# Kernel optimization log

Measured on AMD Instinct MI355X. Metric: run time of the kernel, lower is better.

Reference implementation:

```python
import jax, jax.numpy as jnp
import numpy as np

EPS = 0.5          # entropy_epsilon
TAU = 0.5          # tau = 1 * entropy_epsilon
MAXITER = 10

NABLA_W = np.array([[[[0., 0., 0.], [0., -1., 0.], [0., 1., 0.]]],
                    [[[0., 0., 0.], [0., -1., 1.], [0., 0., 0.]]]], dtype=np.float32)  # (2,1,3,3)
DIV_W = np.array([[[[0., -1., 0.], [0., 1., 0.], [0., 0., 0.]],
                   [[0., 0., 0.], [-1., 1., 0.], [0., 0., 0.]]]], dtype=np.float32)    # (1,2,3,3)


def _conv(x, w):
    # x: (B,C,H,W), w: (O,I,3,3), padding=1 -> SAME
    return jax.lax.conv_general_dilated(
        x, w, window_strides=(1, 1), padding='SAME',
        dimension_numbers=('NCHW', 'OIHW', 'NCHW'))


def setup_inputs() -> dict:
    key = jax.random.key(0)
    k1, k2 = jax.random.split(key)
    B, H, W = 8, 1024, 1024
    o = jax.random.normal(k1, (B, 1, H, W), dtype=jnp.float32)
    vector_field = jax.random.normal(k2, (H, W, 2), dtype=jnp.float32)
    nabla_w = jnp.asarray(NABLA_W)
    div_w = jnp.asarray(DIV_W)
    return {"o": o, "vector_field": vector_field, "nabla_w": nabla_w, "div_w": div_w}


def reference(o, vector_field, nabla_w, div_w):
    o = o[:, 0]                      # (B,H,W)
    vf1 = vector_field[:, :, 1]      # (H,W)
    vf0 = vector_field[:, :, 0]      # (H,W)
    u = jax.nn.sigmoid(o / EPS)
    q = jnp.zeros_like(o)
    Tq = jnp.zeros_like(o)
    for _ in range(MAXITER):
        u_nabla = _conv(u[:, None], nabla_w)          # (B,2,H,W)
        q = q - TAU * (u_nabla[:, 0] * vf1 + u_nabla[:, 1] * vf0)
        q = jnp.maximum(q, 0.0)
        Tq = _conv(jnp.stack([vf1 * q, vf0 * q], axis=1), div_w)[:, 0]  # (B,H,W)
        u = jax.nn.sigmoid((o - Tq) / EPS)
    u1 = (o - Tq) / EPS
    return u1
```

## Files before the change

kernel.cpp:

```cpp
#include <hip/hip_runtime.h>
#include <math.h>

#define IMG_H 1024
#define IMG_W 1024
#define IMG_B 8
#define TPB 1024
#define RPB 16
#define BANDS (IMG_H / RPB)
#define NBLK (IMG_B * BANDS)

__device__ __forceinline__ float sig2(float x) {
    return 1.0f / (1.0f + __expf(-2.0f * x));
}
__device__ __forceinline__ int imax(int a, int b) { return a > b ? a : b; }
__device__ __forceinline__ int imin(int a, int b) { return a < b ? a : b; }

template<int D, bool READQ, bool FINAL>
__global__ __launch_bounds__(TPB, 8) void k_pipe(const float* __restrict__ qin,
                                                 const float* __restrict__ vf,
                                                 const float* __restrict__ o,
                                                 float* __restrict__ out) {
    __shared__ float sp[2][TPB + 1];
    __shared__ float su[D][2][TPB + 1];

    const int img = blockIdx.x / BANDS;
    const int r0  = (blockIdx.x % BANDS) * RPB;
    const int tid = threadIdx.x;
    const size_t ibase = (size_t)img * IMG_H * IMG_W;

    if (tid == 0) {
        sp[0][0] = 0.0f; sp[1][0] = 0.0f;
#pragma unroll
        for (int l = 0; l < D; ++l) { su[l][0][TPB] = 0.0f; su[l][1][TPB] = 0.0f; }
    }

    constexpr int HALO = FINAL ? 1 : 0;
    constexpr int NOH  = FINAL ? D + 1 : D;

    const int u0lo = imax(r0 - (D - 1) - HALO, 0);
    const int ylo  = READQ ? imax(r0 - D - HALO, 0) : u0lo;
    const int yend = r0 + RPB - 1 + D;
    const int yhi  = imin(yend, IMG_H - 1);

    float qc = 0.0f, qz = 0.0f;
    float oh[NOH];
    float v0h[D + 1], v1h[D + 1];
    float uY[D], uZ[D];
    float p1prev[D + 1];
    float qsave[D];
    float qvPrev = 0.0f;

#pragma unroll
    for (int l = 0; l < NOH; ++l) oh[l] = 0.0f;
#pragma unroll
    for (int l = 0; l <= D; ++l) { v0h[l] = 0.0f; v1h[l] = 0.0f; p1prev[l] = 0.0f; }
#pragma unroll
    for (int l = 0; l < D; ++l) { uY[l] = 0.0f; uZ[l] = 0.0f; qsave[l] = 0.0f; }

    const float* pQ = qin + ibase + (size_t)ylo * IMG_W + tid;
    const float* pO = o   + ibase + (size_t)ylo * IMG_W + tid;
    const float* pV = vf  + ((size_t)ylo * IMG_W + tid) * 2;

    for (int y = ylo; y <= yend; ++y) {
#pragma unroll
        for (int k = NOH - 1; k >= 1; --k) oh[k] = oh[k - 1];
#pragma unroll
        for (int k = D; k >= 1; --k) { v0h[k] = v0h[k - 1]; v1h[k] = v1h[k - 1]; }
        if constexpr (READQ) qz = qc;

        if (y <= yhi) {
            if constexpr (READQ) { qc = *pQ; pQ += IMG_W; }
            oh[0] = *pO; pO += IMG_W;
            float2 v2 = *(const float2*)pV; pV += 2 * IMG_W;
            v0h[0] = v2.x; v1h[0] = v2.y;
        } else {
            qc = 0.0f; oh[0] = 0.0f; v0h[0] = 0.0f; v1h[0] = 0.0f;
        }

        if constexpr (READQ) {
            float p0c = v0h[0] * qc;
            float p1c = v1h[0] * qc;
            sp[0][tid + 1] = p0c;
            __syncthreads();
            if (y >= u0lo) {
                float pm1 = sp[0][tid];
                float nu = (y <= IMG_H - 1)
                    ? sig2(oh[0] - (p1c - p1prev[0] + p0c - pm1)) : 0.0f;
                uZ[0] = uY[0]; uY[0] = nu;
                su[0][y & 1][tid] = nu;
            }
            p1prev[0] = p1c;
        } else {
            float nu = (y <= IMG_H - 1) ? sig2(oh[0]) : 0.0f;
            uZ[0] = uY[0]; uY[0] = nu;
            su[0][y & 1][tid] = nu;
        }

#pragma unroll
        for (int l = 1; l <= D; ++l) {
            const int t = y - l;
            const int qlo = imax(r0 - (D - l) - HALO, 0);
            const bool qvalid = (t >= qlo) && (t <= IMG_H - 1);
            float qbase = (l == 1) ? (READQ ? qz : 0.0f) : qsave[l - 1];
            if (l >= 2) qsave[l - 1] = qvPrev;
            float qv;
            if (qvalid) {
                const float uR = su[l - 1][t & 1][tid + 1];
                float gy = uY[l - 1] - uZ[l - 1];
                float gx = uR - uZ[l - 1];
                qv = fmaxf(qbase - 0.5f * (gy * v1h[l] + gx * v0h[l]), 0.0f);
            } else {
                qv = 0.0f;
            }

            if (l < D) {
                float p0p = v0h[l] * qv;
                float p1p = v1h[l] * qv;
                sp[l & 1][tid + 1] = p0p;
                __syncthreads();
                const int ulo = imax(r0 - (D - 1 - l) - HALO, 0);
                if (t >= ulo) {
                    float pm1 = sp[l & 1][tid];
                    float nu = (t <= IMG_H - 1)
                        ? sig2(oh[l] - (p1p - p1prev[l] + p0p - pm1)) : 0.0f;
                    uZ[l] = uY[l]; uY[l] = nu;
                    su[l][t & 1][tid] = nu;
                }
                p1prev[l] = p1p;
            } else {
                if constexpr (FINAL) {
                    float p0p = v0h[D] * qv;
                    float p1p = v1h[D] * qv;
                    sp[D & 1][tid + 1] = p0p;
                    __syncthreads();
                    if (t >= r0 && t < r0 + RPB) {
                        float pm1 = sp[D & 1][tid];
                        float Tq = p1p - p1prev[D] + p0p - pm1;
                        out[ibase + (size_t)t * IMG_W + tid] = 2.0f * (oh[D] - Tq);
                    }
                    p1prev[D] = p1p;
                } else {
                    if (t >= r0 && t < r0 + RPB)
                        out[ibase + (size_t)t * IMG_W + tid] = qv;
                }
            }
            qvPrev = qv;
        }
    }
}

extern "C" void kernel_launch(void* const* d_in, const int* in_sizes, int n_in,
                              void* d_out, int out_size, void* d_ws, size_t ws_size,
                              hipStream_t stream) {
    const float* o  = (const float*)d_in[0];
    const float* vf = (const float*)d_in[1];
    float* qA = (float*)d_ws;

    k_pipe<5, false, false><<<NBLK, TPB, 0, stream>>>(o, vf, o, qA);
    k_pipe<5, true,  true ><<<NBLK, TPB, 0, stream>>>(qA, vf, o, (float*)d_out);
}
```

Baseline: 218.0 us.

## Replace block-wide shared-memory exchange with wavefront-local shuffles over overlapping column strips

Each block now holds two 64-lane wavefronts, and each wavefront covers an overlapping 128-column strip (stride 116, horizontal halo of 6). Neighbour values are exchanged with __shfl_up/__shfl_down instead of shared memory, and each lane handles two pixels with float2/float4 loads. This removes the many __syncthreads per row across a 1024-thread block. The cost is redundant halo computation, about 10% extra work per strip, and more registers per thread.

```diff
diff --git a/kernel.cpp b/kernel.cpp
--- a/kernel.cpp
+++ b/kernel.cpp
@@ -4,10 +4,14 @@
 #define IMG_H 1024
 #define IMG_W 1024
 #define IMG_B 8
-#define TPB 1024
+#define TPB 128
 #define RPB 16
 #define BANDS (IMG_H / RPB)
-#define NBLK (IMG_B * BANDS)
+#define NSTR 9
+#define STRIDE 116
+#define XHALO 6
+#define WPB (TPB / 64)
+#define NBLK (IMG_B * BANDS * NSTR / WPB)
 
 __device__ __forceinline__ float sig2(float x) {
     return 1.0f / (1.0f + __expf(-2.0f * x));
@@ -16,23 +20,22 @@
 __device__ __forceinline__ int imin(int a, int b) { return a < b ? a : b; }
 
 template<int D, bool READQ, bool FINAL>
-__global__ __launch_bounds__(TPB, 8) void k_pipe(const float* __restrict__ qin,
+__global__ __launch_bounds__(TPB, 4) void k_pipe(const float* __restrict__ qin,
                                                  const float* __restrict__ vf,
                                                  const float* __restrict__ o,
                                                  float* __restrict__ out) {
-    __shared__ float sp[2][TPB + 1];
-    __shared__ float su[D][2][TPB + 1];
-
-    const int img = blockIdx.x / BANDS;
-    const int r0  = (blockIdx.x % BANDS) * RPB;
-    const int tid = threadIdx.x;
+    const int gw    = blockIdx.x * WPB + (threadIdx.x >> 6);
+    const int strip = gw % NSTR;
+    const int bg    = gw / NSTR;
+    const int band  = bg % BANDS;
+    const int img   = bg / BANDS;
+    const int lane  = threadIdx.x & 63;
+    const int r0    = band * RPB;
+    const int x     = strip * STRIDE - XHALO + lane * 2;
+    const bool ok   = ((unsigned)x < (unsigned)IMG_W);
+    const int  xc   = imin(imax(x, 0), IMG_W - 2);
+    const bool inter = ok && (lane >= 3) && (lane <= 60);
     const size_t ibase = (size_t)img * IMG_H * IMG_W;
-
-    if (tid == 0) {
-        sp[0][0] = 0.0f; sp[1][0] = 0.0f;
-#pragma unroll
-        for (int l = 0; l < D; ++l) { su[l][0][TPB] = 0.0f; su[l][1][TPB] = 0.0f; }
-    }
 
     constexpr int HALO = FINAL ? 1 : 0;
     constexpr int NOH  = FINAL ? D + 1 : D;
@@ -42,58 +45,77 @@
     const int yend = r0 + RPB - 1 + D;
     const int yhi  = imin(yend, IMG_H - 1);
 
-    float qc = 0.0f, qz = 0.0f;
-    float oh[NOH];
-    float v0h[D + 1], v1h[D + 1];
-    float uY[D], uZ[D];
-    float p1prev[D + 1];
-    float qsave[D];
-    float qvPrev = 0.0f;
+    float qc[2], qz[2], qvPrev[2];
+    float oh[NOH][2];
+    float v0h[D + 1][2], v1h[D + 1][2];
+    float uY[D][2], uZ[D][2];
+    float p1prev[D + 1][2];
+    float qsave[D][2];
 
 #pragma unroll
-    for (int l = 0; l < NOH; ++l) oh[l] = 0.0f;
+    for (int j = 0; j < 2; ++j) {
+        qc[j] = qz[j] = qvPrev[j] = 0.0f;
 #pragma unroll
-    for (int l = 0; l <= D; ++l) { v0h[l] = 0.0f; v1h[l] = 0.0f; p1prev[l] = 0.0f; }
+        for (int l = 0; l < NOH; ++l) oh[l][j] = 0.0f;
 #pragma unroll
-    for (int l = 0; l < D; ++l) { uY[l] = 0.0f; uZ[l] = 0.0f; qsave[l] = 0.0f; }
+        for (int l = 0; l <= D; ++l) { v0h[l][j] = 0.0f; v1h[l][j] = 0.0f; p1prev[l][j] = 0.0f; }
+#pragma unroll
+        for (int l = 0; l < D; ++l) { uY[l][j] = 0.0f; uZ[l][j] = 0.0f; qsave[l][j] = 0.0f; }
+    }
 
-    const float* pQ = qin + ibase + (size_t)ylo * IMG_W + tid;
-    const float* pO = o   + ibase + (size_t)ylo * IMG_W + tid;
-    const float* pV = vf  + ((size_t)ylo * IMG_W + tid) * 2;
+    const float* pQ = qin + ibase + (size_t)ylo * IMG_W + xc;
+    const float* pO = o   + ibase + (size_t)ylo * IMG_W + xc;
+    const float* pV = vf  + ((size_t)ylo * IMG_W + xc) * 2;
 
     for (int y = ylo; y <= yend; ++y) {
 #pragma unroll
-        for (int k = NOH - 1; k >= 1; --k) oh[k] = oh[k - 1];
+        for (int k = NOH - 1; k >= 1; --k) { oh[k][0] = oh[k-1][0]; oh[k][1] = oh[k-1][1]; }
 #pragma unroll
-        for (int k = D; k >= 1; --k) { v0h[k] = v0h[k - 1]; v1h[k] = v1h[k - 1]; }
-        if constexpr (READQ) qz = qc;
+        for (int k = D; k >= 1; --k) {
+            v0h[k][0] = v0h[k-1][0]; v0h[k][1] = v0h[k-1][1];
+            v1h[k][0] = v1h[k-1][0]; v1h[k][1] = v1h[k-1][1];
+        }
+        if constexpr (READQ) { qz[0] = qc[0]; qz[1] = qc[1]; }
 
         if (y <= yhi) {
-            if constexpr (READQ) { qc = *pQ; pQ += IMG_W; }
-            oh[0] = *pO; pO += IMG_W;
-            float2 v2 = *(const float2*)pV; pV += 2 * IMG_W;
-            v0h[0] = v2.x; v1h[0] = v2.y;
+            if constexpr (READQ) {
+                float2 q2 = *(const float2*)pQ; pQ += IMG_W;
+                qc[0] = q2.x; qc[1] = q2.y;
+            }
+            float2 o2 = *(const float2*)pO; pO += IMG_W;
+            oh[0][0] = ok ? o2.x : -1e30f;
+            oh[0][1] = ok ? o2.y : -1e30f;
+            float4 v4 = *(const float4*)pV; pV += 2 * IMG_W;
+            v0h[0][0] = ok ? v4.x : 0.0f;  v1h[0][0] = ok ? v4.y : 0.0f;
+            v0h[0][1] = ok ? v4.z : 0.0f;  v1h[0][1] = ok ? v4.w : 0.0f;
         } else {
-            qc = 0.0f; oh[0] = 0.0f; v0h[0] = 0.0f; v1h[0] = 0.0f;
+            qc[0] = qc[1] = 0.0f;
+            oh[0][0] = oh[0][1] = 0.0f;
+            v0h[0][0] = v0h[0][1] = 0.0f;
+            v1h[0][0] = v1h[0][1] = 0.0f;
         }
 
         if constexpr (READQ) {
-            float p0c = v0h[0] * qc;
-            float p1c = v1h[0] * qc;
-            sp[0][tid + 1] = p0c;
-            __syncthreads();
+            float p0c[2], p1c[2];
+            p0c[0] = v0h[0][0] * qc[0];  p0c[1] = v0h[0][1] * qc[1];
+            p1c[0] = v1h[0][0] * qc[0];  p1c[1] = v1h[0][1] * qc[1];
+            const float pm1 = __shfl_up(p0c[1], 1);
             if (y >= u0lo) {
-                float pm1 = sp[0][tid];
-                float nu = (y <= IMG_H - 1)
-                    ? sig2(oh[0] - (p1c - p1prev[0] + p0c - pm1)) : 0.0f;
-                uZ[0] = uY[0]; uY[0] = nu;
-                su[0][y & 1][tid] = nu;
+#pragma unroll
+                for (int j = 0; j < 2; ++j) {
+                    float pl = (j == 0) ? pm1 : p0c[0];
+                    float arg = oh[0][j] - (p1c[j] - p1prev[0][j] + p0c[j] - pl);
+                    float nu = (y <= IMG_H - 1) ? sig2(arg) : 0.0f;
+                    uZ[0][j] = uY[0][j]; uY[0][j] = nu;
+                }
             }
-            p1prev[0] = p1c;
+            p1prev[0][0] = p1c[0]; p1prev[0][1] = p1c[1];
         } else {
-            float nu = (y <= IMG_H - 1) ? sig2(oh[0]) : 0.0f;
-            uZ[0] = uY[0]; uY[0] = nu;
-            su[0][y & 1][tid] = nu;
+#pragma unroll
+            for (int j = 0; j < 2; ++j) {
+                float nu = (y <= IMG_H - 1) ? sig2(oh[0][j]) : 0.0f;
+                uZ[0][j] = uY[0][j]; uY[0][j] = nu;
+            }
         }
 
 #pragma unroll
@@ -101,50 +123,66 @@
             const int t = y - l;
             const int qlo = imax(r0 - (D - l) - HALO, 0);
             const bool qvalid = (t >= qlo) && (t <= IMG_H - 1);
-            float qbase = (l == 1) ? (READQ ? qz : 0.0f) : qsave[l - 1];
-            if (l >= 2) qsave[l - 1] = qvPrev;
-            float qv;
+            float qb[2], qv[2];
+#pragma unroll
+            for (int j = 0; j < 2; ++j)
+                qb[j] = (l == 1) ? (READQ ? qz[j] : 0.0f) : qsave[l - 1][j];
+            if (l >= 2) { qsave[l - 1][0] = qvPrev[0]; qsave[l - 1][1] = qvPrev[1]; }
+
+            const float uRz = __shfl_down(uZ[l - 1][0], 1);
             if (qvalid) {
-                const float uR = su[l - 1][t & 1][tid + 1];
-                float gy = uY[l - 1] - uZ[l - 1];
-                float gx = uR - uZ[l - 1];
-                qv = fmaxf(qbase - 0.5f * (gy * v1h[l] + gx * v0h[l]), 0.0f);
+#pragma unroll
+                for (int j = 0; j < 2; ++j) {
+                    float gy = uY[l - 1][j] - uZ[l - 1][j];
+                    float gx = ((j == 0) ? uZ[l - 1][1] : uRz) - uZ[l - 1][j];
+                    qv[j] = fmaxf(qb[j] - 0.5f * (gy * v1h[l][j] + gx * v0h[l][j]), 0.0f);
+                }
             } else {
-                qv = 0.0f;
+                qv[0] = 0.0f; qv[1] = 0.0f;
             }
 
             if (l < D) {
-                float p0p = v0h[l] * qv;
-                float p1p = v1h[l] * qv;
-                sp[l & 1][tid + 1] = p0p;
-                __syncthreads();
+                float p0p[2], p1p[2];
+                p0p[0] = v0h[l][0] * qv[0];  p0p[1] = v0h[l][1] * qv[1];
+                p1p[0] = v1h[l][0] * qv[0];  p1p[1] = v1h[l][1] * qv[1];
+                const float pm1 = __shfl_up(p0p[1], 1);
                 const int ulo = imax(r0 - (D - 1 - l) - HALO, 0);
                 if (t >= ulo) {
-                    float pm1 = sp[l & 1][tid];
-                    float nu = (t <= IMG_H - 1)
-                        ? sig2(oh[l] - (p1p - p1prev[l] + p0p - pm1)) : 0.0f;
-                    uZ[l] = uY[l]; uY[l] = nu;
-                    su[l][t & 1][tid] = nu;
+#pragma unroll
+                    for (int j = 0; j < 2; ++j) {
+                        float pl = (j == 0) ? pm1 : p0p[0];
+                        float arg = oh[l][j] - (p1p[j] - p1prev[l][j] + p0p[j] - pl);
+                        float nu = (t <= IMG_H - 1) ? sig2(arg) : 0.0f;
+                        uZ[l][j] = uY[l][j]; uY[l][j] = nu;
+                    }
                 }
-                p1prev[l] = p1p;
+                p1prev[l][0] = p1p[0]; p1prev[l][1] = p1p[1];
             } else {
                 if constexpr (FINAL) {
-                    float p0p = v0h[D] * qv;
-                    float p1p = v1h[D] * qv;
-                    sp[D & 1][tid + 1] = p0p;
-                    __syncthreads();
+                    float p0p[2], p1p[2];
+                    p0p[0] = v0h[D][0] * qv[0];  p0p[1] = v0h[D][1] * qv[1];
+                    p1p[0] = v1h[D][0] * qv[0];  p1p[1] = v1h[D][1] * qv[1];
+                    const float pm1 = __shfl_up(p0p[1], 1);
                     if (t >= r0 && t < r0 + RPB) {
-                        float pm1 = sp[D & 1][tid];
-                        float Tq = p1p - p1prev[D] + p0p - pm1;
-                        out[ibase + (size_t)t * IMG_W + tid] = 2.0f * (oh[D] - Tq);
+                        float r[2];
+#pragma unroll
+                        for (int j = 0; j < 2; ++j) {
+                            float pl = (j == 0) ? pm1 : p0p[0];
+                            float Tq = p1p[j] - p1prev[D][j] + p0p[j] - pl;
+                            r[j] = 2.0f * (oh[D][j] - Tq);
+                        }
+                        if (inter)
+                            *(float2*)(out + ibase + (size_t)t * IMG_W + x) =
+                                make_float2(r[0], r[1]);
                     }
-                    p1prev[D] = p1p;
+                    p1prev[D][0] = p1p[0]; p1prev[D][1] = p1p[1];
                 } else {
-                    if (t >= r0 && t < r0 + RPB)
-                        out[ibase + (size_t)t * IMG_W + tid] = qv;
+                    if (t >= r0 && t < r0 + RPB && inter)
+                        *(float2*)(out + ibase + (size_t)t * IMG_W + x) =
+                            make_float2(qv[0], qv[1]);
                 }
             }
-            qvPrev = qv;
+            qvPrev[0] = qv[0]; qvPrev[1] = qv[1];
         }
     }
 }
```

New measurement: 247.3 us. 13.5% more time.

## Skew wavefront pipeline by two rows to batch barriers per row

Applied to the files above, without the earlier changes.

The per-stage pipeline is restructured so stage l lags by 2*l rows instead of l. All q updates for every stage can then be computed before a single barrier, followed by all u updates and a second barrier. This cuts the per-row barrier count from D+1 to two. In exchange, o and vf are reloaded from global memory per stage instead of kept in shifting register histories, and more rows of pipeline warm-up are added per band.

```diff
diff --git a/kernel.cpp b/kernel.cpp
--- a/kernel.cpp
+++ b/kernel.cpp
@@ -20,7 +20,7 @@
                                                  const float* __restrict__ vf,
                                                  const float* __restrict__ o,
                                                  float* __restrict__ out) {
-    __shared__ float sp[2][TPB + 1];
+    __shared__ float sp[D + 1][TPB + 1];
     __shared__ float su[D][2][TPB + 1];
 
     const int img = blockIdx.x / BANDS;
@@ -29,123 +29,111 @@
     const size_t ibase = (size_t)img * IMG_H * IMG_W;
 
     if (tid == 0) {
-        sp[0][0] = 0.0f; sp[1][0] = 0.0f;
+#pragma unroll
+        for (int l = 0; l <= D; ++l) sp[l][0] = 0.0f;
 #pragma unroll
         for (int l = 0; l < D; ++l) { su[l][0][TPB] = 0.0f; su[l][1][TPB] = 0.0f; }
     }
 
     constexpr int HALO = FINAL ? 1 : 0;
-    constexpr int NOH  = FINAL ? D + 1 : D;
-
     const int u0lo = imax(r0 - (D - 1) - HALO, 0);
     const int ylo  = READQ ? imax(r0 - D - HALO, 0) : u0lo;
-    const int yend = r0 + RPB - 1 + D;
-    const int yhi  = imin(yend, IMG_H - 1);
+    const int yend = r0 + RPB - 1 + 2 * D;
 
-    float qc = 0.0f, qz = 0.0f;
-    float oh[NOH];
-    float v0h[D + 1], v1h[D + 1];
     float uY[D], uZ[D];
     float p1prev[D + 1];
-    float qsave[D];
-    float qvPrev = 0.0f;
+    float qs1[D], qs2[D];
 
 #pragma unroll
-    for (int l = 0; l < NOH; ++l) oh[l] = 0.0f;
+    for (int l = 0; l < D; ++l) { uY[l] = 0.0f; uZ[l] = 0.0f; qs1[l] = 0.0f; qs2[l] = 0.0f; }
 #pragma unroll
-    for (int l = 0; l <= D; ++l) { v0h[l] = 0.0f; v1h[l] = 0.0f; p1prev[l] = 0.0f; }
-#pragma unroll
-    for (int l = 0; l < D; ++l) { uY[l] = 0.0f; uZ[l] = 0.0f; qsave[l] = 0.0f; }
-
-    const float* pQ = qin + ibase + (size_t)ylo * IMG_W + tid;
-    const float* pO = o   + ibase + (size_t)ylo * IMG_W + tid;
-    const float* pV = vf  + ((size_t)ylo * IMG_W + tid) * 2;
+    for (int l = 0; l <= D; ++l) p1prev[l] = 0.0f;
 
     for (int y = ylo; y <= yend; ++y) {
+        float p0s[D + 1], p1s[D + 1], ot[D + 1];
+
+        float qc = 0.0f;
+        {
+            const int yc = imin(y, IMG_H - 1);
+            ot[0] = o[ibase + (size_t)yc * IMG_W + tid];
+            if constexpr (READQ) {
+                const float q0 = qin[ibase + (size_t)yc * IMG_W + tid];
+                const float2 v2 = *(const float2*)(vf + ((size_t)yc * IMG_W + tid) * 2);
+                qc = (y <= IMG_H - 1) ? q0 : 0.0f;
+                p0s[0] = v2.x * qc;
+                p1s[0] = v2.y * qc;
+                sp[0][tid + 1] = p0s[0];
+            }
+        }
+        float qvPrev = 0.0f;
 #pragma unroll
-        for (int k = NOH - 1; k >= 1; --k) oh[k] = oh[k - 1];
-#pragma unroll
-        for (int k = D; k >= 1; --k) { v0h[k] = v0h[k - 1]; v1h[k] = v1h[k - 1]; }
-        if constexpr (READQ) qz = qc;
+        for (int l = 1; l <= D; ++l) {
+            const int t  = y - 2 * l;
+            const int tc = imin(imax(t, 0), IMG_H - 1);
+            const int qlo = imax(r0 - (D - l) - HALO, 0);
+            const bool qvalid = (t >= qlo) && (t <= IMG_H - 1);
 
-        if (y <= yhi) {
-            if constexpr (READQ) { qc = *pQ; pQ += IMG_W; }
-            oh[0] = *pO; pO += IMG_W;
-            float2 v2 = *(const float2*)pV; pV += 2 * IMG_W;
-            v0h[0] = v2.x; v1h[0] = v2.y;
-        } else {
-            qc = 0.0f; oh[0] = 0.0f; v0h[0] = 0.0f; v1h[0] = 0.0f;
+            const float qb = qs2[l - 1];
+            qs2[l - 1] = qs1[l - 1];
+            qs1[l - 1] = (l == 1) ? qc : qvPrev;
+
+            const float2 vt = *(const float2*)(vf + ((size_t)tc * IMG_W + tid) * 2);
+            const float uR = su[l - 1][t & 1][tid + 1];
+            const float gy = uY[l - 1] - uZ[l - 1];
+            const float gx = uR - uZ[l - 1];
+            const float qv = qvalid
+                ? fmaxf(qb - 0.5f * (gy * vt.y + gx * vt.x), 0.0f) : 0.0f;
+
+            if (l < D || FINAL) {
+                p0s[l] = vt.x * qv;
+                p1s[l] = vt.y * qv;
+                sp[l][tid + 1] = p0s[l];
+                ot[l] = o[ibase + (size_t)tc * IMG_W + tid];
+            } else {
+                if (t >= r0 && t < r0 + RPB)
+                    out[ibase + (size_t)t * IMG_W + tid] = qv;
+            }
+            qvPrev = qv;
         }
+        __syncthreads();
 
         if constexpr (READQ) {
-            float p0c = v0h[0] * qc;
-            float p1c = v1h[0] * qc;
-            sp[0][tid + 1] = p0c;
-            __syncthreads();
             if (y >= u0lo) {
-                float pm1 = sp[0][tid];
-                float nu = (y <= IMG_H - 1)
-                    ? sig2(oh[0] - (p1c - p1prev[0] + p0c - pm1)) : 0.0f;
+                const float pm1 = sp[0][tid];
+                const float nu = (y <= IMG_H - 1)
+                    ? sig2(ot[0] - (p1s[0] - p1prev[0] + p0s[0] - pm1)) : 0.0f;
                 uZ[0] = uY[0]; uY[0] = nu;
                 su[0][y & 1][tid] = nu;
             }
-            p1prev[0] = p1c;
+            p1prev[0] = p1s[0];
         } else {
-            float nu = (y <= IMG_H - 1) ? sig2(oh[0]) : 0.0f;
+            const float nu = (y <= IMG_H - 1) ? sig2(ot[0]) : 0.0f;
             uZ[0] = uY[0]; uY[0] = nu;
             su[0][y & 1][tid] = nu;
         }
-
 #pragma unroll
-        for (int l = 1; l <= D; ++l) {
-            const int t = y - l;
-            const int qlo = imax(r0 - (D - l) - HALO, 0);
-            const bool qvalid = (t >= qlo) && (t <= IMG_H - 1);
-            float qbase = (l == 1) ? (READQ ? qz : 0.0f) : qsave[l - 1];
-            if (l >= 2) qsave[l - 1] = qvPrev;
-            float qv;
-            if (qvalid) {
-                const float uR = su[l - 1][t & 1][tid + 1];
-                float gy = uY[l - 1] - uZ[l - 1];
-                float gx = uR - uZ[l - 1];
-                qv = fmaxf(qbase - 0.5f * (gy * v1h[l] + gx * v0h[l]), 0.0f);
-            } else {
-                qv = 0.0f;
+        for (int l = 1; l < D; ++l) {
+            const int t = y - 2 * l;
+            const int ulo = imax(r0 - (D - 1 - l) - HALO, 0);
+            if (t >= ulo) {
+                const float pm1 = sp[l][tid];
+                const float nu = (t <= IMG_H - 1)
+                    ? sig2(ot[l] - (p1s[l] - p1prev[l] + p0s[l] - pm1)) : 0.0f;
+                uZ[l] = uY[l]; uY[l] = nu;
+                su[l][t & 1][tid] = nu;
             }
-
-            if (l < D) {
-                float p0p = v0h[l] * qv;
-                float p1p = v1h[l] * qv;
-                sp[l & 1][tid + 1] = p0p;
-                __syncthreads();
-                const int ulo = imax(r0 - (D - 1 - l) - HALO, 0);
-                if (t >= ulo) {
-                    float pm1 = sp[l & 1][tid];
-                    float nu = (t <= IMG_H - 1)
-                        ? sig2(oh[l] - (p1p - p1prev[l] + p0p - pm1)) : 0.0f;
-                    uZ[l] = uY[l]; uY[l] = nu;
-                    su[l][t & 1][tid] = nu;
-                }
-                p1prev[l] = p1p;
-            } else {
-                if constexpr (FINAL) {
-                    float p0p = v0h[D] * qv;
-                    float p1p = v1h[D] * qv;
-                    sp[D & 1][tid + 1] = p0p;
-                    __syncthreads();
-                    if (t >= r0 && t < r0 + RPB) {
-                        float pm1 = sp[D & 1][tid];
-                        float Tq = p1p - p1prev[D] + p0p - pm1;
-                        out[ibase + (size_t)t * IMG_W + tid] = 2.0f * (oh[D] - Tq);
-                    }
-                    p1prev[D] = p1p;
-                } else {
-                    if (t >= r0 && t < r0 + RPB)
-                        out[ibase + (size_t)t * IMG_W + tid] = qv;
-                }
+            p1prev[l] = p1s[l];
+        }
+        if constexpr (FINAL) {
+            const int t = y - 2 * D;
+            if (t >= r0 && t < r0 + RPB) {
+                const float pm1 = sp[D][tid];
+                const float Tq = p1s[D] - p1prev[D] + p0s[D] - pm1;
+                out[ibase + (size_t)t * IMG_W + tid] = 2.0f * (ot[D] - Tq);
             }
-            qvPrev = qv;
+            p1prev[D] = p1s[D];
         }
+        __syncthreads();
     }
 }
 
```

Measured after the change: 284.3 us. 30.4% more time.

## Process two pixels per thread with 512-thread blocks and packed float2 math

Applied to the files above, without the earlier changes.

Each thread now handles two adjacent columns, so blocks use 512 threads covering a full 1024-wide row. Loads and stores become float2/float4 and the arithmetic uses 2-wide vectors, which may map to packed FP32 instructions. The shared-memory exchange carries only the edge value per thread, and each pipeline stage gets its own sp buffer. Fewer threads per barrier and wider memory accesses are meant to cut sync and instruction overhead, at the cost of more registers per thread and half the number of threads.

```diff
diff --git a/kernel.cpp b/kernel.cpp
--- a/kernel.cpp
+++ b/kernel.cpp
@@ -4,10 +4,13 @@
 #define IMG_H 1024
 #define IMG_W 1024
 #define IMG_B 8
-#define TPB 1024
+#define TPB 512
+#define PXT 2
 #define RPB 16
 #define BANDS (IMG_H / RPB)
 #define NBLK (IMG_B * BANDS)
+
+typedef float v2f __attribute__((ext_vector_type(2)));
 
 __device__ __forceinline__ float sig2(float x) {
     return 1.0f / (1.0f + __expf(-2.0f * x));
@@ -16,20 +19,22 @@
 __device__ __forceinline__ int imin(int a, int b) { return a < b ? a : b; }
 
 template<int D, bool READQ, bool FINAL>
-__global__ __launch_bounds__(TPB, 8) void k_pipe(const float* __restrict__ qin,
+__global__ __launch_bounds__(TPB, 4) void k_pipe(const float* __restrict__ qin,
                                                  const float* __restrict__ vf,
                                                  const float* __restrict__ o,
                                                  float* __restrict__ out) {
-    __shared__ float sp[2][TPB + 1];
+    __shared__ float sp[D + 1][TPB + 1];
     __shared__ float su[D][2][TPB + 1];
 
     const int img = blockIdx.x / BANDS;
     const int r0  = (blockIdx.x % BANDS) * RPB;
     const int tid = threadIdx.x;
+    const int x0  = tid * PXT;
     const size_t ibase = (size_t)img * IMG_H * IMG_W;
 
     if (tid == 0) {
-        sp[0][0] = 0.0f; sp[1][0] = 0.0f;
+#pragma unroll
+        for (int l = 0; l <= D; ++l) sp[l][0] = 0.0f;
 #pragma unroll
         for (int l = 0; l < D; ++l) { su[l][0][TPB] = 0.0f; su[l][1][TPB] = 0.0f; }
     }
@@ -42,24 +47,24 @@
     const int yend = r0 + RPB - 1 + D;
     const int yhi  = imin(yend, IMG_H - 1);
 
-    float qc = 0.0f, qz = 0.0f;
-    float oh[NOH];
-    float v0h[D + 1], v1h[D + 1];
-    float uY[D], uZ[D];
-    float p1prev[D + 1];
-    float qsave[D];
-    float qvPrev = 0.0f;
+    const v2f z2 = {0.0f, 0.0f};
+    v2f qc = z2, qz = z2, qvPrev = z2;
+    v2f oh[NOH];
+    v2f v0h[D + 1], v1h[D + 1];
+    v2f uY[D], uZ[D];
+    v2f p1prev[D + 1];
+    v2f qsave[D];
 
 #pragma unroll
-    for (int l = 0; l < NOH; ++l) oh[l] = 0.0f;
+    for (int l = 0; l < NOH; ++l) oh[l] = z2;
 #pragma unroll
-    for (int l = 0; l <= D; ++l) { v0h[l] = 0.0f; v1h[l] = 0.0f; p1prev[l] = 0.0f; }
+    for (int l = 0; l <= D; ++l) { v0h[l] = z2; v1h[l] = z2; p1prev[l] = z2; }
 #pragma unroll
-    for (int l = 0; l < D; ++l) { uY[l] = 0.0f; uZ[l] = 0.0f; qsave[l] = 0.0f; }
+    for (int l = 0; l < D; ++l) { uY[l] = z2; uZ[l] = z2; qsave[l] = z2; }
 
-    const float* pQ = qin + ibase + (size_t)ylo * IMG_W + tid;
-    const float* pO = o   + ibase + (size_t)ylo * IMG_W + tid;
-    const float* pV = vf  + ((size_t)ylo * IMG_W + tid) * 2;
+    const float* pQ = qin + ibase + (size_t)ylo * IMG_W + x0;
+    const float* pO = o   + ibase + (size_t)ylo * IMG_W + x0;
+    const float* pV = vf  + ((size_t)ylo * IMG_W + x0) * 2;
 
     for (int y = ylo; y <= yend; ++y) {
 #pragma unroll
@@ -69,31 +74,41 @@
         if constexpr (READQ) qz = qc;
 
         if (y <= yhi) {
-            if constexpr (READQ) { qc = *pQ; pQ += IMG_W; }
-            oh[0] = *pO; pO += IMG_W;
-            float2 v2 = *(const float2*)pV; pV += 2 * IMG_W;
-            v0h[0] = v2.x; v1h[0] = v2.y;
+            if constexpr (READQ) {
+                float2 q2 = *(const float2*)pQ; pQ += IMG_W;
+                qc = (v2f){q2.x, q2.y};
+            }
+            float2 o2 = *(const float2*)pO; pO += IMG_W;
+            oh[0] = (v2f){o2.x, o2.y};
+            float4 v4 = *(const float4*)pV; pV += 2 * IMG_W;
+            v0h[0] = (v2f){v4.x, v4.z};
+            v1h[0] = (v2f){v4.y, v4.w};
         } else {
-            qc = 0.0f; oh[0] = 0.0f; v0h[0] = 0.0f; v1h[0] = 0.0f;
+            qc = z2; oh[0] = z2; v0h[0] = z2; v1h[0] = z2;
         }
 
         if constexpr (READQ) {
-            float p0c = v0h[0] * qc;
-            float p1c = v1h[0] * qc;
-            sp[0][tid + 1] = p0c;
+            v2f p0c = v0h[0] * qc;
+            v2f p1c = v1h[0] * qc;
+            sp[0][tid + 1] = p0c.y;
             __syncthreads();
             if (y >= u0lo) {
-                float pm1 = sp[0][tid];
-                float nu = (y <= IMG_H - 1)
-                    ? sig2(oh[0] - (p1c - p1prev[0] + p0c - pm1)) : 0.0f;
+                const float lft = sp[0][tid];
+                v2f pl = {lft, p0c.x};
+                v2f ar = oh[0] - (p1c - p1prev[0] + p0c - pl);
+                v2f nu;
+                if (y <= IMG_H - 1) { nu.x = sig2(ar.x); nu.y = sig2(ar.y); }
+                else                  nu = z2;
                 uZ[0] = uY[0]; uY[0] = nu;
-                su[0][y & 1][tid] = nu;
+                su[0][y & 1][tid] = nu.x;
             }
             p1prev[0] = p1c;
         } else {
-            float nu = (y <= IMG_H - 1) ? sig2(oh[0]) : 0.0f;
+            v2f nu;
+            if (y <= IMG_H - 1) { nu.x = sig2(oh[0].x); nu.y = sig2(oh[0].y); }
+            else                  nu = z2;
             uZ[0] = uY[0]; uY[0] = nu;
-            su[0][y & 1][tid] = nu;
+            su[0][y & 1][tid] = nu.x;
         }
 
 #pragma unroll
@@ -101,47 +116,58 @@
             const int t = y - l;
             const int qlo = imax(r0 - (D - l) - HALO, 0);
             const bool qvalid = (t >= qlo) && (t <= IMG_H - 1);
-            float qbase = (l == 1) ? (READQ ? qz : 0.0f) : qsave[l - 1];
+            v2f qb = (l == 1) ? (READQ ? qz : z2) : qsave[l - 1];
             if (l >= 2) qsave[l - 1] = qvPrev;
-            float qv;
+            v2f qv;
             if (qvalid) {
-                const float uR = su[l - 1][t & 1][tid + 1];
-                float gy = uY[l - 1] - uZ[l - 1];
-                float gx = uR - uZ[l - 1];
-                qv = fmaxf(qbase - 0.5f * (gy * v1h[l] + gx * v0h[l]), 0.0f);
+                const float uRx = su[l - 1][t & 1][tid + 1];
+                v2f uR = {uZ[l - 1].y, uRx};
+                v2f gy = uY[l - 1] - uZ[l - 1];
+                v2f gx = uR - uZ[l - 1];
+                v2f s  = gy * v1h[l] + gx * v0h[l];
+                v2f c  = qb - 0.5f * s;
+                qv.x = fmaxf(c.x, 0.0f);
+                qv.y = fmaxf(c.y, 0.0f);
             } else {
-                qv = 0.0f;
+                qv = z2;
             }
 
             if (l < D) {
-                float p0p = v0h[l] * qv;
-                float p1p = v1h[l] * qv;
-                sp[l & 1][tid + 1] = p0p;
+                v2f p0p = v0h[l] * qv;
+                v2f p1p = v1h[l] * qv;
+                sp[l][tid + 1] = p0p.y;
                 __syncthreads();
                 const int ulo = imax(r0 - (D - 1 - l) - HALO, 0);
                 if (t >= ulo) {
-                    float pm1 = sp[l & 1][tid];
-                    float nu = (t <= IMG_H - 1)
-                        ? sig2(oh[l] - (p1p - p1prev[l] + p0p - pm1)) : 0.0f;
+                    const float lft = sp[l][tid];
+                    v2f pl = {lft, p0p.x};
+                    v2f ar = oh[l] - (p1p - p1prev[l] + p0p - pl);
+                    v2f nu;
+                    if (t <= IMG_H - 1) { nu.x = sig2(ar.x); nu.y = sig2(ar.y); }
+                    else                  nu = z2;
                     uZ[l] = uY[l]; uY[l] = nu;
-                    su[l][t & 1][tid] = nu;
+                    su[l][t & 1][tid] = nu.x;
                 }
                 p1prev[l] = p1p;
             } else {
                 if constexpr (FINAL) {
-                    float p0p = v0h[D] * qv;
-                    float p1p = v1h[D] * qv;
-                    sp[D & 1][tid + 1] = p0p;
+                    v2f p0p = v0h[D] * qv;
+                    v2f p1p = v1h[D] * qv;
+                    sp[D][tid + 1] = p0p.y;
                     __syncthreads();
                     if (t >= r0 && t < r0 + RPB) {
-                        float pm1 = sp[D & 1][tid];
-                        float Tq = p1p - p1prev[D] + p0p - pm1;
-                        out[ibase + (size_t)t * IMG_W + tid] = 2.0f * (oh[D] - Tq);
+                        const float lft = sp[D][tid];
+                        v2f pl = {lft, p0p.x};
+                        v2f Tq = p1p - p1prev[D] + p0p - pl;
+                        v2f r  = 2.0f * (oh[D] - Tq);
+                        *(float2*)(out + ibase + (size_t)t * IMG_W + x0) =
+                            make_float2(r.x, r.y);
                     }
                     p1prev[D] = p1p;
                 } else {
                     if (t >= r0 && t < r0 + RPB)
-                        out[ibase + (size_t)t * IMG_W + tid] = qv;
+                        *(float2*)(out + ibase + (size_t)t * IMG_W + x0) =
+                            make_float2(qv.x, qv.y);
                 }
             }
             qvPrev = qv;
```

New measurement: 222.8 us. 2.2% more time.
